# Optimization experiments

Measured on AMD Instinct MI355X. Metric: run time of the kernel, lower is better.

Reference implementation:

```python
import jax, jax.numpy as jnp
import numpy as np

NN, NB = 100_000, 20_000          # note / beat node counts
IN_C, HID, OUT_C = 64, 128, 32
NUM_LAYERS = 3
EPS_LN = 1e-5
EPS_BN = 1e-5


def setup_inputs() -> dict:
    key = jax.random.key(0)
    ks = jax.random.split(key, 24)

    def edges(k, ne, ns, nd):
        k1, k2 = jax.random.split(k)
        src = jax.random.randint(k1, (ne,), 0, ns)
        dst = jax.random.randint(k2, (ne,), 0, nd)
        return jnp.stack([src, dst]).astype(jnp.int64)

    p = lambda k, shp: jax.random.normal(k, shp, dtype=jnp.float32) * 0.05
    return {
        "x_note": jax.random.normal(ks[0], (NN, IN_C), dtype=jnp.float32),
        "x_beat": jax.random.normal(ks[1], (NB, IN_C), dtype=jnp.float32),
        "e_onset": edges(ks[2], 800_000, NN, NN),
        "e_consec": edges(ks[3], 300_000, NN, NN),
        "e_nb": edges(ks[4], 100_000, NN, NB),   # note -> beat
        "e_bn": edges(ks[5], 100_000, NB, NN),   # beat -> note
        "e_bb": edges(ks[6], 20_000, NB, NB),
        "proj_W": p(ks[7], (5, IN_C, IN_C)),
        "proj_b": jnp.zeros((5, IN_C), jnp.float32),
        "l0_Wl": p(ks[8], (5, IN_C, HID)),
        "l0_bl": jnp.zeros((5, HID), jnp.float32),
        "l0_Wr": p(ks[9], (5, IN_C, HID)),
        "Wl": p(ks[10], (NUM_LAYERS - 1, 5, HID, HID)),
        "bl": jnp.zeros((NUM_LAYERS - 1, 5, HID), jnp.float32),
        "Wr": p(ks[11], (NUM_LAYERS - 1, 5, HID, HID)),
        "ln_g": jnp.ones((NUM_LAYERS - 1, HID), jnp.float32),
        "ln_b": jnp.zeros((NUM_LAYERS - 1, HID), jnp.float32),
        "mlp_W1": p(ks[12], (HID, HID)),
        "mlp_b1": jnp.zeros((HID,), jnp.float32),
        "bn_g": jnp.ones((HID,), jnp.float32),
        "bn_b": jnp.zeros((HID,), jnp.float32),
        "mlp_W2": p(ks[13], (HID, OUT_C)),
        "mlp_b2": jnp.zeros((OUT_C,), jnp.float32),
    }


def _seg_mean(msg, dst, n):
    s = jax.ops.segment_sum(msg, dst, num_segments=n)
    c = jax.ops.segment_sum(jnp.ones((dst.shape[0], 1), msg.dtype), dst, num_segments=n)
    return s / jnp.maximum(c, 1.0)


def _l2norm(x):  # F.normalize(p=2, dim=-1)
    return x / jnp.maximum(jnp.linalg.norm(x, axis=-1, keepdims=True), 1e-12)


def _ln(x, g, b):
    m = x.mean(-1, keepdims=True)
    v = ((x - m) ** 2).mean(-1, keepdims=True)
    return (x - m) / jnp.sqrt(v + EPS_LN) * g + b


def reference(x_note, x_beat, e_onset, e_consec, e_nb, e_bn, e_bb,
              proj_W, proj_b, l0_Wl, l0_bl, l0_Wr, Wl, bl, Wr,
              ln_g, ln_b, mlp_W1, mlp_b1, bn_g, bn_b, mlp_W2, mlp_b2):
    x = {"note": x_note, "beat": x_beat}
    sizes = {"note": x_note.shape[0], "beat": x_beat.shape[0]}
    # (relation_idx, src_type, dst_type, edge_index[2,E])
    rels = [(0, "note", "note", e_onset), (1, "note", "note", e_consec),
            (2, "note", "beat", e_nb), (3, "beat", "note", e_bn),
            (4, "beat", "beat", e_bb)]

    for i in range(NUM_LAYERS):
        outs = {"note": [], "beat": []}
        for r, s, d, e in rels:
            xs, xd = x[s], x[d]
            if i == 0:  # SAGEConv(project=True, normalize=True)
                xs = jax.nn.relu(xs @ proj_W[r] + proj_b[r])
                W_l, b_l, W_r = l0_Wl[r], l0_bl[r], l0_Wr[r]
            else:
                W_l, b_l, W_r = Wl[i - 1, r], bl[i - 1, r], Wr[i - 1, r]
            agg = _seg_mean(xs[e[0]], e[1], sizes[d])       # gather -> mean scatter
            o = agg @ W_l + b_l + xd @ W_r                   # lin_l(agg) + lin_r(x_dst)
            if i == 0:
                o = _l2norm(o)
            outs[d].append(o)
        # HeteroConv aggr='mean' across relations per dst type
        x = {k: jnp.mean(jnp.stack(v), axis=0) for k, v in outs.items()}
        if i != NUM_LAYERS - 1:  # relu -> LayerNorm -> dropout(eval: identity)
            x = {k: _ln(jax.nn.relu(v), ln_g[i], ln_b[i]) for k, v in x.items()}

    note = x["note"]
    h = jax.nn.relu(note @ mlp_W1 + mlp_b1)
    # BatchNorm1d eval mode with running stats (mean=0, var=1)
    h = h / jnp.sqrt(1.0 + EPS_BN) * bn_g + bn_b
    return h @ mlp_W2 + mlp_b2
```

## Files before the change

### kernel.cpp

```cpp
#include <hip/hip_runtime.h>
#include <math.h>

typedef unsigned int   u32;
typedef unsigned short u16;
typedef short   short8 __attribute__((ext_vector_type(8)));
typedef float   f32x4  __attribute__((ext_vector_type(4)));

constexpr int NN = 100000;
constexpr int NB = 20000;
constexpr int LTOT = 3 * NN + 2 * NB;

__device__ inline float blo(u32 u) { union { u32 i; float f; } v; v.i = u << 16;        return v.f; }
__device__ inline float bhi(u32 u) { union { u32 i; float f; } v; v.i = u & 0xffff0000u; return v.f; }
__device__ inline u16  f2b(float f)
{ union { float f; u32 u; } v; v.f = f; return (u16)((v.u + 0x7fffu + ((v.u >> 16) & 1u)) >> 16); }

template<int K1, int K2, int C, int EPI, bool BIAS>
__global__ __launch_bounds__(256)
void gemm16_k(const u16* __restrict__ A1, const u16* __restrict__ A2,
              const u16* __restrict__ W, const float* __restrict__ bias,
              const float* __restrict__ g, const float* __restrict__ bvec,
              float scale, float* __restrict__ Yf, u16* __restrict__ Yh, int n)
{
    constexpr int K   = K1 + K2;
    constexpr int NKB = K / 64;
    constexpr int WVN = (C >= 64) ? 2 : 1;
    constexpr int WVM = 4 / WVN;
    constexpr int RT2 = 2;
    constexpr int BM  = WVM * RT2 * 16;
    constexpr int CT  = C / (WVN * 16);
    static_assert(K1 % 64 == 0 && (K2 == 0 || K2 % 64 == 0), "K multiple of 64");

    __shared__ uint4 sA[BM * 8];
    __shared__ uint4 sW[C * 8];
    __shared__ float redS[2][BM];
    __shared__ float redQ[2][BM];

    const int tid  = threadIdx.x;
    const int lane = tid & 63;
    const int wv   = tid >> 6;
    const int wm   = wv % WVM;
    const int wn   = wv / WVM;
    const int lrow = lane & 15;
// ... 2 lines not shown

    f32x4 acc[RT2][CT];
    #pragma unroll
    for (int rt = 0; rt < RT2; ++rt)
        #pragma unroll
        for (int ct = 0; ct < CT; ++ct) acc[rt][ct] = (f32x4){0.f, 0.f, 0.f, 0.f};

    for (int kb = 0; kb < NKB; ++kb) {
        if (kb) __syncthreads();
        const bool useA1 = (K2 == 0) || (kb * 64 < K1);
        {
            const u16* Asel   = useA1 ? A1 : A2;
            const int astride = useA1 ? K1 : K2;
            const int aoff    = useA1 ? kb * 64 : kb * 64 - K1;
            for (int u = tid; u < BM * 8; u += 256) {
                const int r  = u >> 3, k8 = u & 7;
                const int row = row0 + r;
                uint4 v = make_uint4(0u, 0u, 0u, 0u);
                if (row < n)
                    v = *reinterpret_cast<const uint4*>(Asel + (size_t)row * astride + aoff + k8 * 8);
                sA[(r * 8 + k8) ^ (r & 7)] = v;
            }
        }
        {
            u16* sWu = (u16*)sW;
            for (int u = tid; u < 64 * (C / 8); u += 256) {
                const int kk = u & 63, c8 = (u >> 6) * 8;
                const uint4 v = *reinterpret_cast<const uint4*>(W + (size_t)(kb * 64 + kk) * C + c8);
                const u16* e = (const u16*)&v;
                #pragma unroll
                for (int j = 0; j < 8; ++j) {
                    const int c = c8 + j;
                    sWu[(c * 64 + kk) ^ ((c & 7) << 3)] = e[j];
                }
            }
        }
        __syncthreads();
        #pragma unroll
        for (int ks = 0; ks < 2; ++ks) {
            short8 af[RT2];
            #pragma unroll
            for (int rt = 0; rt < RT2; ++rt) {
                const int r = (wm * RT2 + rt) * 16 + lrow;
                af[rt] = *reinterpret_cast<const short8*>(&sA[(r * 8 + ks * 4 + lk8) ^ (lrow & 7)]);
            }
            #pragma unroll
            for (int ct = 0; ct < CT; ++ct) {
                const int c = (wn * CT + ct) * 16 + lrow;
                const short8 bfr = *reinterpret_cast<const short8*>(&sW[(c * 8 + ks * 4 + lk8) ^ (lrow & 7)]);
                #pragma unroll
                for (int rt = 0; rt < RT2; ++rt)
                    acc[rt][ct] = __builtin_amdgcn_mfma_f32_16x16x32_bf16(af[rt], bfr, acc[rt][ct], 0, 0, 0);
            }
        }
    }

    float vals[RT2][CT][4];
    #pragma unroll
    for (int ct = 0; ct < CT; ++ct) {
        const int colg = (wn * CT + ct) * 16 + lrow;
        const float bs = BIAS ? bias[colg] : 0.f;
        #pragma unroll
        for (int rt = 0; rt < RT2; ++rt)
            #pragma unroll
            for (int r = 0; r < 4; ++r) {
                float v = acc[rt][ct][r] + bs;
                if (EPI == 2 || EPI == 5) v = fmaxf(v, 0.f);
                vals[rt][ct][r] = v;
            }
    }

    if (EPI <= 2) {
        #pragma unroll
        for (int ct = 0; ct < CT; ++ct) {
            const int colg = (wn * CT + ct) * 16 + lrow;
            #pragma unroll
            for (int rt = 0; rt < RT2; ++rt) {
                const int rbase = row0 + (wm * RT2 + rt) * 16 + lk8 * 4;
                #pragma unroll
                for (int r = 0; r < 4; ++r) {
                    const int row = rbase + r;
                    if (row >= n) continue;
                    if (EPI == 0) Yf[(size_t)row * C + colg] = vals[rt][ct][r];
                    else          Yh[(size_t)row * C + colg] = f2b(vals[rt][ct][r]);
                }
            }
        }
    } else {
        #pragma unroll
        for (int rt = 0; rt < RT2; ++rt)
            #pragma unroll
            for (int r = 0; r < 4; ++r) {
                float pS = 0.f, pQ = 0.f;
                #pragma unroll
                for (int ct = 0; ct < CT; ++ct) { const float v = vals[rt][ct][r]; pS += v; pQ += v * v; }
                #pragma unroll
                for (int m = 1; m <= 8; m <<= 1) {
                    pS += __shfl_xor(pS, m, 64);
                    pQ += __shfl_xor(pQ, m, 64);
                }
                if (lrow == 0) {
                    const int rowl = (wm * RT2 + rt) * 16 + lk8 * 4 + r;
                    redS[wn][rowl] = pS; redQ[wn][rowl] = pQ;
                }
            }
        __syncthreads();
        #pragma unroll
        for (int rt = 0; rt < RT2; ++rt)
            #pragma unroll
            for (int r = 0; r < 4; ++r) {
                const int rowl = (wm * RT2 + rt) * 16 + lk8 * 4 + r;
// ... 3 lines not shown
                    const float ss  = redQ[0][rowl] + redQ[1][rowl];
                    const float inv = scale / fmaxf(sqrtf(ss), 1e-12f);
                    #pragma unroll
                    for (int ct = 0; ct < CT; ++ct) {
                        const int colg = (wn * CT + ct) * 16 + lrow;
                        float o = vals[rt][ct][r] * inv;
                        if (EPI == 4) o += Yf[(size_t)row * C + colg];
                        Yf[(size_t)row * C + colg] = o;
                    }
                } else {
                    const float S = redS[0][rowl] + redS[1][rowl];
                    const float Q = redQ[0][rowl] + redQ[1][rowl];
                    const float mean = S * (1.0f / C);
                    const float var  = Q * (1.0f / C) - mean * mean;
                    const float inv  = 1.0f / sqrtf(var + 1e-5f);
                    #pragma unroll
                    for (int ct = 0; ct < CT; ++ct) {
                        const int colg = (wn * CT + ct) * 16 + lrow;
                        const float o = (vals[rt][ct][r] - mean) * inv * g[colg] + bvec[colg];
                        Yh[(size_t)row * C + colg] = f2b(o);
                    }
                }
            }
    }
}

struct Rels { const int* e[5]; int E[5]; int rowoff[5]; };

__global__ __launch_bounds__(256)
void hist_all_k(Rels R, int* __restrict__ deg)
{
    const int ri = blockIdx.y;
    const int e = blockIdx.x * 256 + threadIdx.x;
    if (e < R.E[ri]) atomicAdd(&deg[R.rowoff[ri] + R.e[ri][e + R.E[ri]]], 1);
}

__global__ __launch_bounds__(256)
void fill_all_k(Rels R, const int* __restrict__ rowptr, int* __restrict__ next,
                int* __restrict__ colsrc)
{
    const int ri = blockIdx.y;
    const int e = blockIdx.x * 256 + threadIdx.x;
    if (e >= R.E[ri]) return;
    const int s = R.e[ri][e], d = R.e[ri][e + R.E[ri]];
    const int p = atomicAdd(&next[R.rowoff[ri] + d], 1);
    colsrc[rowptr[R.rowoff[ri] + d] + p] = s;
// ... 38 lines not shown
    #pragma unroll
    for (int off = 1; off < 64; off <<= 1) {
        const int u = __shfl_up(sc, off, 64);
        if ((tid & 63) >= off) sc += u;
    }
    if ((tid & 63) == 63) ws[tid >> 6] = sc;
    __syncthreads();
    int add = 0;
    for (int i = 0; i < (tid >> 6); ++i) add += ws[i];
    if (tid < nb) bsum[tid] = sc + add;
}

__global__ __launch_bounds__(256)
void scan3_k(int* __restrict__ rowptr, const int* __restrict__ bsum, int n)
{
    const int i = blockIdx.x * 256 + threadIdx.x;
    if (i == 0) rowptr[0] = 0;
    if (i < n) {
        const int b = i >> 11;
        if (b > 0) rowptr[i + 1] += bsum[b - 1];
    }
}

__global__ __launch_bounds__(256)
void agg128_k(const u16* __restrict__ X, const int* __restrict__ rowptr,
              const int* __restrict__ colsrc, int rowoff, int n, float scale,
              u16* __restrict__ out, int rs, int co)
{
    const int wid  = (int)((blockIdx.x * 256 + threadIdx.x) >> 6);
    const int lane = threadIdx.x & 63;
    if (wid >= n) return;
    const int beg = rowptr[rowoff + wid], end = rowptr[rowoff + wid + 1];
    const int sub = lane >> 5, cl = lane & 31;
    const uint2* X2 = (const uint2*)X;
    float a0 = 0.f, a1 = 0.f, a2 = 0.f, a3 = 0.f;
    int j = beg + sub;
    for (; j + 2 < end; j += 4) {
        const int s0 = colsrc[j], s1 = colsrc[j + 2];
        const uint2 v0 = X2[(size_t)s0 * 32 + cl];
        const uint2 v1 = X2[(size_t)s1 * 32 + cl];
        a0 += blo(v0.x) + blo(v1.x); a1 += bhi(v0.x) + bhi(v1.x);
        a2 += blo(v0.y) + blo(v1.y); a3 += bhi(v0.y) + bhi(v1.y);
    }
    for (; j < end; j += 2) {
        const uint2 v = X2[(size_t)colsrc[j] * 32 + cl];
        a0 += blo(v.x); a1 += bhi(v.x); a2 += blo(v.y); a3 += bhi(v.y);
    }
    a0 += __shfl_xor(a0, 32, 64); a1 += __shfl_xor(a1, 32, 64);
    a2 += __shfl_xor(a2, 32, 64); a3 += __shfl_xor(a3, 32, 64);
    if (sub == 0) {
        const float m = scale / fmaxf((float)(end - beg), 1.0f);
        uint2 p;
        p.x = (u32)f2b(a0 * m) | ((u32)f2b(a1 * m) << 16);
        p.y = (u32)f2b(a2 * m) | ((u32)f2b(a3 * m) << 16);
        ((uint2*)(out + (size_t)wid * rs + co))[cl] = p;
    }
}

__global__ __launch_bounds__(256)
void agg64_k(const u16* __restrict__ X, const int* __restrict__ rowptr,
             const int* __restrict__ colsrc, int rowoff, int n, float scale,
             u16* __restrict__ out)
{
    const int wid  = (int)((blockIdx.x * 256 + threadIdx.x) >> 6);
    const int lane = threadIdx.x & 63;
    if (wid >= n) return;
    const int beg = rowptr[rowoff + wid], end = rowptr[rowoff + wid + 1];
    const int sub = lane >> 5, cl = lane & 31;
    const u32* X1 = (const u32*)X;
    float a0 = 0.f, a1 = 0.f;
    int j = beg + sub;
    for (; j + 2 < end; j += 4) {
        const u32 v0 = X1[(size_t)colsrc[j] * 32 + cl];
        const u32 v1 = X1[(size_t)colsrc[j + 2] * 32 + cl];
        a0 += blo(v0) + blo(v1); a1 += bhi(v0) + bhi(v1);
    }
    for (; j < end; j += 2) {
        const u32 v = X1[(size_t)colsrc[j] * 32 + cl];
        a0 += blo(v); a1 += bhi(v);
    }
    a0 += __shfl_xor(a0, 32, 64); a1 += __shfl_xor(a1, 32, 64);
    if (sub == 0) {
        const float m = scale / fmaxf((float)(end - beg), 1.0f);
        ((u32*)(out + (size_t)wid * 64))[cl] = (u32)f2b(a0 * m) | ((u32)f2b(a1 * m) << 16);
    }
}

__global__ __launch_bounds__(256)
void relu_ln16_k(const float* __restrict__ X, const float* __restrict__ g,
                 const float* __restrict__ b, u16* __restrict__ OUT, int n)
{
    const int wid  = (int)((blockIdx.x * 256 + threadIdx.x) >> 6);
    const int lane = threadIdx.x & 63;
    if (wid >= n) return;
    const float* x = X + (size_t)wid * 128;
    const float v0 = fmaxf(x[lane], 0.f), v1 = fmaxf(x[lane + 64], 0.f);
    float s = v0 + v1;
    #pragma unroll
    for (int off = 32; off > 0; off >>= 1) s += __shfl_xor(s, off, 64);
    const float m  = s * (1.0f / 128.0f);
    const float d0 = v0 - m, d1 = v1 - m;
    float vv = d0 * d0 + d1 * d1;
    #pragma unroll
    for (int off = 32; off > 0; off >>= 1) vv += __shfl_xor(vv, off, 64);
    const float inv = 1.0f / sqrtf(vv * (1.0f / 128.0f) + 1e-5f);
    OUT[(size_t)wid * 128 + lane]      = f2b(d0 * inv * g[lane]      + b[lane]);
    OUT[(size_t)wid * 128 + lane + 64] = f2b(d1 * inv * g[lane + 64] + b[lane + 64]);
}

__global__ void l0wcat_k(const float* __restrict__ Wl, const float* __restrict__ Wr,
                         u16* __restrict__ out)
{
    const int r = blockIdx.y;
    const int idx = blockIdx.x * 256 + threadIdx.x;
    const int row = idx >> 7, c = idx & 127;
    const float v = (row < 64) ? Wl[(size_t)r * 8192 + row * 128 + c]
                               : Wr[(size_t)r * 8192 + (row - 64) * 128 + c];
    out[(size_t)r * 16384 + idx] = f2b(v);
}

__global__ void wcat_k(const float* __restrict__ Wl, const float* __restrict__ Wr,
                       const float* __restrict__ bl, u16* __restrict__ WcatN,
                       u16* __restrict__ WcatB, float* __restrict__ bcatN,
                       float* __restrict__ bcatB)
{
    const int job = blockIdx.y;
    const int idx = blockIdx.x * 256 + threadIdx.x;
    if (job < 2) {
        const int li = job;
        const float* WlL = Wl + (size_t)li * 5 * 16384;
        const float* WrL = Wr + (size_t)li * 5 * 16384;
        if (idx < 512 * 128) {
            const int row = idx >> 7, c = idx & 127;
            float v;
            if (row < 384) {
                const int rsel = row >> 7;
                const int rel = (rsel == 2) ? 3 : rsel;
                v = WlL[(size_t)rel * 16384 + (row & 127) * 128 + c];
            } else {
                const int rr = row - 384;
                v = (WrL[(size_t)0 * 16384 + rr * 128 + c] + WrL[(size_t)1 * 16384 + rr * 128 + c]
                   + WrL[(size_t)3 * 16384 + rr * 128 + c]) * (1.0f / 3.0f);
            }
            WcatN[(size_t)li * 512 * 128 + idx] = f2b(v);
        }
        if (blockIdx.x == 0 && threadIdx.x < 128) {
            const float* blL = bl + (size_t)li * 5 * 128;
            bcatN[li * 128 + threadIdx.x] =
                (blL[threadIdx.x] + blL[128 + threadIdx.x] + blL[3 * 128 + threadIdx.x]) * (1.0f / 3.0f);
        }
    } else {
        if (idx < 384 * 128) {
            const int row = idx >> 7, c = idx & 127;
            float v;
            if (row < 256) {
                const int rel = (row < 128) ? 2 : 4;
                v = Wl[(size_t)rel * 16384 + (row & 127) * 128 + c];
            } else {
                const int rr = row - 256;
                v = (Wr[(size_t)2 * 16384 + rr * 128 + c] + Wr[(size_t)4 * 16384 + rr * 128 + c]) * 0.5f;
            }
            WcatB[idx] = f2b(v);
        }
        if (blockIdx.x == 0 && threadIdx.x < 128)
            bcatB[threadIdx.x] = (bl[2 * 128 + threadIdx.x] + bl[4 * 128 + threadIdx.x]) * 0.5f;
    }
}

__global__ void headprep_k(const float* __restrict__ W2, const float* __restrict__ b2,
                           const float* __restrict__ bng, const float* __restrict__ bnb,
                           u16* __restrict__ W2p16, float* __restrict__ b2p)
{
    const int idx = blockIdx.x * 256 + threadIdx.x;
    const float is = 1.0f / sqrtf(1.0f + 1e-5f);
    if (idx < 128 * 32) {
        const int k = idx >> 5;
        W2p16[idx] = f2b(W2[idx] * (bng[k] * is));
    }
    if (idx < 32) {
        float s = b2[idx];
        for (int k = 0; k < 128; ++k) s += bnb[k] * W2[k * 32 + idx];
        b2p[idx] = s;
    }
}

struct CastJobs { const float* s[4]; u16* d[4]; int n[4]; };
__global__ __launch_bounds__(256)
void castmany_k(CastJobs J)
{
    const int j = blockIdx.y;
    const float* s = J.s[j]; u16* d = J.d[j]; const int n = J.n[j];
    for (int i = blockIdx.x * 256 + threadIdx.x; i < n; i += gridDim.x * 256)
        d[i] = f2b(s[i]);
}

extern "C" void kernel_launch(void* const* d_in, const int* in_sizes, int n_in,
                              void* d_out, int out_size, void* d_ws, size_t ws_size,
                              hipStream_t stream)
{
    (void)n_in; (void)out_size; (void)ws_size;

    const float* x_note = (const float*)d_in[0];
    const float* x_beat = (const float*)d_in[1];
    const int*   e_on   = (const int*)d_in[2];
    const int*   e_co   = (const int*)d_in[3];
    const int*   e_nb   = (const int*)d_in[4];
    const int*   e_bn   = (const int*)d_in[5];
    const int*   e_bb   = (const int*)d_in[6];
    const float* proj_W = (const float*)d_in[7];
    const float* proj_b = (const float*)d_in[8];
    const float* l0_Wl  = (const float*)d_in[9];
    const float* l0_bl  = (const float*)d_in[10];
    const float* l0_Wr  = (const float*)d_in[11];
    const float* Wl     = (const float*)d_in[12];
    const float* bl     = (const float*)d_in[13];
    const float* Wr     = (const float*)d_in[14];
    const float* ln_g   = (const float*)d_in[15];
    const float* ln_b   = (const float*)d_in[16];
    const float* W1     = (const float*)d_in[17];
    const float* b1     = (const float*)d_in[18];
    const float* bn_g   = (const float*)d_in[19];
    const float* bn_b   = (const float*)d_in[20];
    const float* W2     = (const float*)d_in[21];
    const float* b2     = (const float*)d_in[22];

    const int E_on = in_sizes[2] / 2, E_co = in_sizes[3] / 2, E_nb = in_sizes[4] / 2,
              E_bn = in_sizes[5] / 2, E_bb = in_sizes[6] / 2;
    const int ETOT = E_on + E_co + E_nb + E_bn + E_bb;

    char* wsb = (char*)d_ws;
    size_t off = 0;
    auto alloc = [&](size_t bytes) { char* p = wsb + off; off += (bytes + 255) & ~(size_t)255; return p; };
    float* nF    = (float*)alloc((size_t)NN * 128 * 4);
    float* bF    = (float*)alloc((size_t)NB * 128 * 4);
    u16*  n16    = (u16*)alloc((size_t)NN * 128 * 2);
    u16*  b16    = (u16*)alloc((size_t)NB * 128 * 2);
    u16*  agg16  = (u16*)alloc((size_t)NN * 384 * 2);
    u16*  aggB   = (u16*)alloc((size_t)NB * 256 * 2);
    u16*  xn16   = n16;
    u16*  xb16   = b16;
    u16*  n16h   = (u16*)nF;
    u16*  proj16 = agg16 + (size_t)NN * 64;
    u16*  tmp16h = agg16;
    u16*  projW16 = (u16*)alloc(5 * 64 * 64 * 2);
    u16*  l0Wc16  = (u16*)alloc(5 * 128 * 128 * 2);
    u16*  WcatN   = (u16*)alloc(2 * 512 * 128 * 2);
    u16*  WcatB   = (u16*)alloc(384 * 128 * 2);
    u16*  W116    = (u16*)alloc(128 * 128 * 2);
    u16*  W2p16   = (u16*)alloc(128 * 32 * 2);
    float* bcatN  = (float*)alloc(2 * 128 * 4);
    float* bcatB  = (float*)alloc(128 * 4);
    float* b2p    = (float*)alloc(32 * 4);
    int* rowptr = (int*)alloc((LTOT + 64) * 4);
    int* deg    = (int*)alloc(LTOT * 4);
    int* colsrc = (int*)alloc((size_t)ETOT * 4);
    int* bsum   = (int*)alloc(256 * 4);

    Rels R;
    R.e[0] = e_on; R.e[1] = e_co; R.e[2] = e_nb; R.e[3] = e_bn; R.e[4] = e_bb;
    R.E[0] = E_on; R.E[1] = E_co; R.E[2] = E_nb; R.E[3] = E_bn; R.E[4] = E_bb;
    R.rowoff[0] = 0; R.rowoff[1] = NN; R.rowoff[2] = 2 * NN;
    R.rowoff[3] = 2 * NN + NB; R.rowoff[4] = 3 * NN + NB;
    int maxE = E_on;
    for (int i = 1; i < 5; ++i) if (R.E[i] > maxE) maxE = R.E[i];

    hipMemsetAsync(deg, 0, (size_t)LTOT * 4, stream);
    hist_all_k<<<dim3((maxE + 255) / 256, 5), 256, 0, stream>>>(R, deg);
    const int NBLK = (LTOT + 2047) / 2048;
    scan1_k<<<NBLK, 256, 0, stream>>>(deg, rowptr, bsum, LTOT);
    scan2p_k<<<1, 256, 0, stream>>>(bsum, NBLK);
    scan3_k<<<(LTOT + 255) / 256, 256, 0, stream>>>(rowptr, bsum, LTOT);
    hipMemsetAsync(deg, 0, (size_t)LTOT * 4, stream);
    fill_all_k<<<dim3((maxE + 255) / 256, 5), 256, 0, stream>>>(R, rowptr, deg, colsrc);

    l0wcat_k<<<dim3(64, 5), 256, 0, stream>>>(l0_Wl, l0_Wr, l0Wc16);
    wcat_k<<<dim3(256, 3), 256, 0, stream>>>(Wl, Wr, bl, WcatN, WcatB, bcatN, bcatB);
    headprep_k<<<16, 256, 0, stream>>>(W2, b2, bn_g, bn_b, W2p16, b2p);
    {
        CastJobs J;
        J.s[0] = x_note; J.d[0] = xn16;    J.n[0] = NN * 64;
        J.s[1] = x_beat; J.d[1] = xb16;    J.n[1] = NB * 64;
        J.s[2] = proj_W; J.d[2] = projW16; J.n[2] = 5 * 64 * 64;
        J.s[3] = W1;     J.d[3] = W116;    J.n[3] = 128 * 128;
        castmany_k<<<dim3(512, 4), 256, 0, stream>>>(J);
    }

    const int nsz[2] = {NN, NB};
    const int  relS[5] = {0, 0, 0, 1, 1};
    const int  relD[5] = {0, 0, 1, 0, 1};
    const float Rdiv[2] = {3.0f, 2.0f};

    for (int ri = 0; ri < 5; ++ri) {
        const u16* xs = relS[ri] == 0 ? xn16 : xb16;
        const u16* xd = relD[ri] == 0 ? xn16 : xb16;
        const int ns = nsz[relS[ri]], nd = nsz[relD[ri]];
        float* accum = relD[ri] == 0 ? nF : bF;
        const float sc = 1.0f / Rdiv[relD[ri]];
        gemm16_k<64, 0, 64, 2, true><<<(ns + 63) / 64, 256, 0, stream>>>(
            xs, nullptr, projW16 + (size_t)ri * 4096, proj_b + ri * 64,
            nullptr, nullptr, 0.f, nullptr, proj16, ns);
        agg64_k<<<(nd + 3) / 4, 256, 0, stream>>>(proj16, rowptr, colsrc, R.rowoff[ri], nd, 1.0f, agg16);
        if (ri == 0 || ri == 2)
            gemm16_k<64, 64, 128, 3, true><<<(nd + 63) / 64, 256, 0, stream>>>(
                agg16, xd, l0Wc16 + (size_t)ri * 16384, l0_bl + ri * 128,
                nullptr, nullptr, sc, accum, nullptr, nd);
        else
            gemm16_k<64, 64, 128, 4, true><<<(nd + 63) / 64, 256, 0, stream>>>(
                agg16, xd, l0Wc16 + (size_t)ri * 16384, l0_bl + ri * 128,
                nullptr, nullptr, sc, accum, nullptr, nd);
    }
    relu_ln16_k<<<(NN + 3) / 4, 256, 0, stream>>>(nF, ln_g, ln_b, n16, NN);
    relu_ln16_k<<<(NB + 3) / 4, 256, 0, stream>>>(bF, ln_g, ln_b, b16, NB);

    agg128_k<<<(NN + 3) / 4, 256, 0, stream>>>(n16, rowptr, colsrc, 0,            NN, 1.0f / 3.0f, agg16, 384, 0);
    agg128_k<<<(NN + 3) / 4, 256, 0, stream>>>(n16, rowptr, colsrc, NN,           NN, 1.0f / 3.0f, agg16, 384, 128);
    agg128_k<<<(NN + 3) / 4, 256, 0, stream>>>(b16, rowptr, colsrc, 2 * NN + NB,  NN, 1.0f / 3.0f, agg16, 384, 256);
    agg128_k<<<(NB + 3) / 4, 256, 0, stream>>>(n16, rowptr, colsrc, 2 * NN,       NB, 0.5f,        aggB, 256, 0);
    agg128_k<<<(NB + 3) / 4, 256, 0, stream>>>(b16, rowptr, colsrc, 3 * NN + NB,  NB, 0.5f,        aggB, 256, 128);
    gemm16_k<384, 128, 128, 5, true><<<(NN + 63) / 64, 256, 0, stream>>>(
        agg16, n16, WcatN, bcatN, ln_g + 128, ln_b + 128, 0.f, nullptr, n16, NN);
    gemm16_k<256, 128, 128, 5, true><<<(NB + 63) / 64, 256, 0, stream>>>(
        aggB, b16, WcatB, bcatB, ln_g + 128, ln_b + 128, 0.f, nullptr, b16, NB);

    agg128_k<<<(NN + 3) / 4, 256, 0, stream>>>(n16, rowptr, colsrc, 0,            NN, 1.0f / 3.0f, agg16, 384, 0);
    agg128_k<<<(NN + 3) / 4, 256, 0, stream>>>(n16, rowptr, colsrc, NN,           NN, 1.0f / 3.0f, agg16, 384, 128);
    agg128_k<<<(NN + 3) / 4, 256, 0, stream>>>(b16, rowptr, colsrc, 2 * NN + NB,  NN, 1.0f / 3.0f, agg16, 384, 256);
    gemm16_k<384, 128, 128, 1, true><<<(NN + 63) / 64, 256, 0, stream>>>(
        agg16, n16, WcatN + 512 * 128, bcatN + 128, nullptr, nullptr, 0.f, nullptr, n16h, NN);

    gemm16_k<128, 0, 128, 2, true><<<(NN + 63) / 64, 256, 0, stream>>>(
        n16h, nullptr, W116, b1, nullptr, nullptr, 0.f, nullptr, tmp16h, NN);
    gemm16_k<128, 0, 32, 0, true><<<(NN + 127) / 128, 256, 0, stream>>>(
        tmp16h, nullptr, W2p16, b2p, nullptr, nullptr, 0.f, (float*)d_out, nullptr, NN);
}
```

Measured before the change: 913.2 us.

## Pre-swizzle weights, batch projections and aggregations, fuse relu+LayerNorm into GEMM epilogue

Weights are pre-swizzled once into the shared-memory layout, so the GEMM loads B tiles with plain 16-byte copies instead of scattered 2-byte stores. The per-relation layer-0 projections are merged into one wide GEMM per source type. All per-relation aggregations of a layer now run as a single multi-job kernel instead of separate launches. A new epilogue folds L2-normalise, accumulate, relu and LayerNorm into the last layer-0 GEMM, which removes the standalone relu_ln passes. The trade-off is more launch-table indexing inside the aggregation kernel and a heavier epilogue with extra barriers.

Result: slower. 938.8 us (+2.8%).

```diff
diff --git a/kernel.cpp b/kernel.cpp
--- a/kernel.cpp
+++ b/kernel.cpp
@@ -18,7 +18,7 @@
 template<int K1, int K2, int C, int EPI, bool BIAS>
 __global__ __launch_bounds__(256)
 void gemm16_k(const u16* __restrict__ A1, const u16* __restrict__ A2,
-              const u16* __restrict__ W, const float* __restrict__ bias,
+              const uint4* __restrict__ Wsw, const float* __restrict__ bias,
               const float* __restrict__ g, const float* __restrict__ bvec,
               float scale, float* __restrict__ Yf, u16* __restrict__ Yh, int n)
 {
@@ -67,19 +67,8 @@
                 sA[(r * 8 + k8) ^ (r & 7)] = v;
             }
         }
-        {
-            u16* sWu = (u16*)sW;
-            for (int u = tid; u < 64 * (C / 8); u += 256) {
-                const int kk = u & 63, c8 = (u >> 6) * 8;
-                const uint4 v = *reinterpret_cast<const uint4*>(W + (size_t)(kb * 64 + kk) * C + c8);
-                const u16* e = (const u16*)&v;
-                #pragma unroll
-                for (int j = 0; j < 8; ++j) {
-                    const int c = c8 + j;
-                    sWu[(c * 64 + kk) ^ ((c & 7) << 3)] = e[j];
-                }
-            }
-        }
+        for (int u = tid; u < C * 8; u += 256)
+            sW[u] = Wsw[(size_t)kb * C * 8 + u];
         __syncthreads();
         #pragma unroll
         for (int ks = 0; ks < 2; ++ks) {
@@ -92,7 +81,7 @@
             #pragma unroll
             for (int ct = 0; ct < CT; ++ct) {
                 const int c = (wn * CT + ct) * 16 + lrow;
-                const short8 bfr = *reinterpret_cast<const short8*>(&sW[(c * 8 + ks * 4 + lk8) ^ (lrow & 7)]);
+                const short8 bfr = *reinterpret_cast<const short8*>(&sW[(c * 8 + ks * 4 + lk8) ^ (c & 7)]);
                 #pragma unroll
                 for (int rt = 0; rt < RT2; ++rt)
                     acc[rt][ct] = __builtin_amdgcn_mfma_f32_16x16x32_bf16(af[rt], bfr, acc[rt][ct], 0, 0, 0);
@@ -131,7 +120,7 @@
                 }
             }
         }
-    } else {
+    } else if (EPI == 3 || EPI == 4 || EPI == 5) {
         #pragma unroll
         for (int rt = 0; rt < RT2; ++rt)
             #pragma unroll
@@ -181,6 +170,73 @@
                     }
                 }
             }
+    } else {
+        #pragma unroll
+        for (int rt = 0; rt < RT2; ++rt)
+            #pragma unroll
+            for (int r = 0; r < 4; ++r) {
+                float pQ = 0.f;
+                #pragma unroll
+                for (int ct = 0; ct < CT; ++ct) { const float v = vals[rt][ct][r]; pQ += v * v; }
+                #pragma unroll
+                for (int m = 1; m <= 8; m <<= 1) pQ += __shfl_xor(pQ, m, 64);
+                if (lrow == 0) redQ[wn][(wm * RT2 + rt) * 16 + lk8 * 4 + r] = pQ;
+            }
+        __syncthreads();
+        #pragma unroll
+        for (int rt = 0; rt < RT2; ++rt)
+            #pragma unroll
+            for (int r = 0; r < 4; ++r) {
+                const int rowl = (wm * RT2 + rt) * 16 + lk8 * 4 + r;
+                const int row = row0 + rowl;
+                const float ss  = redQ[0][rowl] + redQ[1][rowl];
+                const float inv = scale / fmaxf(sqrtf(ss), 1e-12f);
+                #pragma unroll
+                for (int ct = 0; ct < CT; ++ct) {
+                    const int colg = (wn * CT + ct) * 16 + lrow;
+                    float o = vals[rt][ct][r] * inv;
+                    if (row < n) o += Yf[(size_t)row * C + colg];
+                    vals[rt][ct][r] = fmaxf(o, 0.f);
+                }
+            }
+        __syncthreads();
+        #pragma unroll
+        for (int rt = 0; rt < RT2; ++rt)
+            #pragma unroll
+            for (int r = 0; r < 4; ++r) {
+                float pS = 0.f, pQ = 0.f;
+                #pragma unroll
+                for (int ct = 0; ct < CT; ++ct) { const float v = vals[rt][ct][r]; pS += v; pQ += v * v; }
+                #pragma unroll
+                for (int m = 1; m <= 8; m <<= 1) {
+                    pS += __shfl_xor(pS, m, 64);
+                    pQ += __shfl_xor(pQ, m, 64);
+                }
+                if (lrow == 0) {
+                    const int rowl = (wm * RT2 + rt) * 16 + lk8 * 4 + r;
+                    redS[wn][rowl] = pS; redQ[wn][rowl] = pQ;
+                }
+            }
+        __syncthreads();
+        #pragma unroll
+        for (int rt = 0; rt < RT2; ++rt)
+            #pragma unroll
+            for (int r = 0; r < 4; ++r) {
+                const int rowl = (wm * RT2 + rt) * 16 + lk8 * 4 + r;
+                const int row = row0 + rowl;
+                if (row >= n) continue;
+                const float S = redS[0][rowl] + redS[1][rowl];
+                const float Q = redQ[0][rowl] + redQ[1][rowl];
+                const float mean = S * (1.0f / C);
+                const float var  = Q * (1.0f / C) - mean * mean;
+                const float inv  = 1.0f / sqrtf(var + 1e-5f);
+                #pragma unroll
+                for (int ct = 0; ct < CT; ++ct) {
+                    const int colg = (wn * CT + ct) * 16 + lrow;
+                    const float o = (vals[rt][ct][r] - mean) * inv * g[colg] + bvec[colg];
+                    Yh[(size_t)row * C + colg] = f2b(o);
+                }
+            }
     }
 }
 
@@ -265,176 +321,186 @@
     }
 }
 
-__global__ __launch_bounds__(256)
-void agg128_k(const u16* __restrict__ X, const int* __restrict__ rowptr,
-              const int* __restrict__ colsrc, int rowoff, int n, float scale,
-              u16* __restrict__ out, int rs, int co)
-{
-    const int wid  = (int)((blockIdx.x * 256 + threadIdx.x) >> 6);
+struct AggJobs {
+    const u16* X[5];
+    u16* out[5];
+    int in_rs[5], in_co[5], rowoff[5], nrows[5], out_rs[5], out_co[5];
+    float scale[5];
+    int pfx[6];
+    int njobs;
+};
+
+template<int C>
+__global__ __launch_bounds__(256)
+void aggm_k(AggJobs J, const int* __restrict__ rowptr, const int* __restrict__ colsrc)
+{
+    const int bid = blockIdx.x;
+    int j = 0;
+    while (j + 1 < J.njobs && bid >= J.pfx[j + 1]) ++j;
+    const int wid = (bid - J.pfx[j]) * 4 + (int)(threadIdx.x >> 6);
+    if (wid >= J.nrows[j]) return;
     const int lane = threadIdx.x & 63;
-    if (wid >= n) return;
-    const int beg = rowptr[rowoff + wid], end = rowptr[rowoff + wid + 1];
     const int sub = lane >> 5, cl = lane & 31;
-    const uint2* X2 = (const uint2*)X;
-    float a0 = 0.f, a1 = 0.f, a2 = 0.f, a3 = 0.f;
-    int j = beg + sub;
-    for (; j + 2 < end; j += 4) {
-        const int s0 = colsrc[j], s1 = colsrc[j + 2];
-        const uint2 v0 = X2[(size_t)s0 * 32 + cl];
-        const uint2 v1 = X2[(size_t)s1 * 32 + cl];
-        a0 += blo(v0.x) + blo(v1.x); a1 += bhi(v0.x) + bhi(v1.x);
-        a2 += blo(v0.y) + blo(v1.y); a3 += bhi(v0.y) + bhi(v1.y);
-    }
-    for (; j < end; j += 2) {
-        const uint2 v = X2[(size_t)colsrc[j] * 32 + cl];
-        a0 += blo(v.x); a1 += bhi(v.x); a2 += blo(v.y); a3 += bhi(v.y);
-    }
-    a0 += __shfl_xor(a0, 32, 64); a1 += __shfl_xor(a1, 32, 64);
-    a2 += __shfl_xor(a2, 32, 64); a3 += __shfl_xor(a3, 32, 64);
-    if (sub == 0) {
-        const float m = scale / fmaxf((float)(end - beg), 1.0f);
-        uint2 p;
-        p.x = (u32)f2b(a0 * m) | ((u32)f2b(a1 * m) << 16);
-        p.y = (u32)f2b(a2 * m) | ((u32)f2b(a3 * m) << 16);
-        ((uint2*)(out + (size_t)wid * rs + co))[cl] = p;
-    }
-}
-
-__global__ __launch_bounds__(256)
-void agg64_k(const u16* __restrict__ X, const int* __restrict__ rowptr,
-             const int* __restrict__ colsrc, int rowoff, int n, float scale,
-             u16* __restrict__ out)
-{
-    const int wid  = (int)((blockIdx.x * 256 + threadIdx.x) >> 6);
-    const int lane = threadIdx.x & 63;
-    if (wid >= n) return;
-    const int beg = rowptr[rowoff + wid], end = rowptr[rowoff + wid + 1];
-    const int sub = lane >> 5, cl = lane & 31;
-    const u32* X1 = (const u32*)X;
-    float a0 = 0.f, a1 = 0.f;
-    int j = beg + sub;
-    for (; j + 2 < end; j += 4) {
-        const u32 v0 = X1[(size_t)colsrc[j] * 32 + cl];
-        const u32 v1 = X1[(size_t)colsrc[j + 2] * 32 + cl];
-        a0 += blo(v0) + blo(v1); a1 += bhi(v0) + bhi(v1);
-    }
-    for (; j < end; j += 2) {
-        const u32 v = X1[(size_t)colsrc[j] * 32 + cl];
-        a0 += blo(v); a1 += bhi(v);
-    }
-    a0 += __shfl_xor(a0, 32, 64); a1 += __shfl_xor(a1, 32, 64);
-    if (sub == 0) {
-        const float m = scale / fmaxf((float)(end - beg), 1.0f);
-        ((u32*)(out + (size_t)wid * 64))[cl] = (u32)f2b(a0 * m) | ((u32)f2b(a1 * m) << 16);
-    }
-}
-
-__global__ __launch_bounds__(256)
-void relu_ln16_k(const float* __restrict__ X, const float* __restrict__ g,
-                 const float* __restrict__ b, u16* __restrict__ OUT, int n)
-{
-    const int wid  = (int)((blockIdx.x * 256 + threadIdx.x) >> 6);
-    const int lane = threadIdx.x & 63;
-    if (wid >= n) return;
-    const float* x = X + (size_t)wid * 128;
-    const float v0 = fmaxf(x[lane], 0.f), v1 = fmaxf(x[lane + 64], 0.f);
-    float s = v0 + v1;
+    const int beg = rowptr[J.rowoff[j] + wid], end = rowptr[J.rowoff[j] + wid + 1];
+    const u16* X = J.X[j];
+    const int irs = J.in_rs[j], ico = J.in_co[j];
+    const float m = J.scale[j] / fmaxf((float)(end - beg), 1.0f);
+    if (C == 128) {
+        float a0 = 0.f, a1 = 0.f, a2 = 0.f, a3 = 0.f;
+        int i = beg + sub;
+        for (; i + 2 < end; i += 4) {
+            const int s0 = colsrc[i], s1 = colsrc[i + 2];
+            const uint2 v0 = *reinterpret_cast<const uint2*>(X + (size_t)s0 * irs + ico + cl * 4);
+            const uint2 v1 = *reinterpret_cast<const uint2*>(X + (size_t)s1 * irs + ico + cl * 4);
+            a0 += blo(v0.x) + blo(v1.x); a1 += bhi(v0.x) + bhi(v1.x);
+            a2 += blo(v0.y) + blo(v1.y); a3 += bhi(v0.y) + bhi(v1.y);
+        }
+        for (; i < end; i += 2) {
+            const uint2 v = *reinterpret_cast<const uint2*>(X + (size_t)colsrc[i] * irs + ico + cl * 4);
+            a0 += blo(v.x); a1 += bhi(v.x); a2 += blo(v.y); a3 += bhi(v.y);
+        }
+        a0 += __shfl_xor(a0, 32, 64); a1 += __shfl_xor(a1, 32, 64);
+        a2 += __shfl_xor(a2, 32, 64); a3 += __shfl_xor(a3, 32, 64);
+        if (sub == 0) {
+            uint2 p;
+            p.x = (u32)f2b(a0 * m) | ((u32)f2b(a1 * m) << 16);
+            p.y = (u32)f2b(a2 * m) | ((u32)f2b(a3 * m) << 16);
+            *reinterpret_cast<uint2*>(J.out[j] + (size_t)wid * J.out_rs[j] + J.out_co[j] + cl * 4) = p;
+        }
+    } else {
+        float a0 = 0.f, a1 = 0.f;
+        int i = beg + sub;
+        for (; i + 2 < end; i += 4) {
+            const u32 v0 = *reinterpret_cast<const u32*>(X + (size_t)colsrc[i] * irs + ico + cl * 2);
+            const u32 v1 = *reinterpret_cast<const u32*>(X + (size_t)colsrc[i + 2] * irs + ico + cl * 2);
+            a0 += blo(v0) + blo(v1); a1 += bhi(v0) + bhi(v1);
+        }
+        for (; i < end; i += 2) {
+            const u32 v = *reinterpret_cast<const u32*>(X + (size_t)colsrc[i] * irs + ico + cl * 2);
+            a0 += blo(v); a1 += bhi(v);
+        }
+        a0 += __shfl_xor(a0, 32, 64); a1 += __shfl_xor(a1, 32, 64);
+        if (sub == 0)
+            *reinterpret_cast<u32*>(J.out[j] + (size_t)wid * J.out_rs[j] + J.out_co[j] + cl * 2) =
+                (u32)f2b(a0 * m) | ((u32)f2b(a1 * m) << 16);
+    }
+}
+
+__global__ __launch_bounds__(256)
+void wprep_k(const float* __restrict__ proj_W, const float* __restrict__ l0_Wl,
+             const float* __restrict__ l0_Wr, const float* __restrict__ Wl,
+             const float* __restrict__ Wr, const float* __restrict__ W1,
+             const float* __restrict__ W2, const float* __restrict__ bn_g,
+             uint4* __restrict__ projNsw, uint4* __restrict__ projBsw,
+             uint4* __restrict__ l0Wsw, uint4* __restrict__ WcatNsw,
+             uint4* __restrict__ WcatBsw, uint4* __restrict__ W1sw,
+             uint4* __restrict__ W2sw)
+{
+    const int job = blockIdx.y;
+    const int t = blockIdx.x * 256 + threadIdx.x;
+    int K, C; uint4* dst;
+    switch (job) {
+        case 0:  K = 64;  C = 192; dst = projNsw; break;
+        case 1:  K = 64;  C = 128; dst = projBsw; break;
+        case 2: case 3: case 4: case 5: case 6:
+                 K = 128; C = 128; dst = l0Wsw + (size_t)(job - 2) * 2048; break;
+        case 7: case 8:
+                 K = 512; C = 128; dst = WcatNsw + (size_t)(job - 7) * 8192; break;
+        case 9:  K = 384; C = 128; dst = WcatBsw; break;
+        case 10: K = 128; C = 128; dst = W1sw; break;
+        default: K = 128; C = 32;  dst = W2sw; break;
+    }
+    if (t >= K * C / 8) return;
+    const int kb = t / (C * 8);
+    const int rem = t % (C * 8);
+    const int c = rem >> 3, k8 = rem & 7;
+    const int k0 = kb * 64 + k8 * 8;
+    const float is = 1.0f / sqrtf(1.0f + 1e-5f);
+    u16 e[8];
     #pragma unroll
-    for (int off = 32; off > 0; off >>= 1) s += __shfl_xor(s, off, 64);
-    const float m  = s * (1.0f / 128.0f);
-    const float d0 = v0 - m, d1 = v1 - m;
-    float vv = d0 * d0 + d1 * d1;
-    #pragma unroll
-    for (int off = 32; off > 0; off >>= 1) vv += __shfl_xor(vv, off, 64);
-    const float inv = 1.0f / sqrtf(vv * (1.0f / 128.0f) + 1e-5f);
-    OUT[(size_t)wid * 128 + lane]      = f2b(d0 * inv * g[lane]      + b[lane]);
-    OUT[(size_t)wid * 128 + lane + 64] = f2b(d1 * inv * g[lane + 64] + b[lane + 64]);
-}
-
-__global__ void l0wcat_k(const float* __restrict__ Wl, const float* __restrict__ Wr,
-                         u16* __restrict__ out)
-{
-    const int r = blockIdx.y;
-    const int idx = blockIdx.x * 256 + threadIdx.x;
-    const int row = idx >> 7, c = idx & 127;
-    const float v = (row < 64) ? Wl[(size_t)r * 8192 + row * 128 + c]
-                               : Wr[(size_t)r * 8192 + (row - 64) * 128 + c];
-    out[(size_t)r * 16384 + idx] = f2b(v);
-}
-
-__global__ void wcat_k(const float* __restrict__ Wl, const float* __restrict__ Wr,
-                       const float* __restrict__ bl, u16* __restrict__ WcatN,
-                       u16* __restrict__ WcatB, float* __restrict__ bcatN,
-                       float* __restrict__ bcatB)
-{
-    const int job = blockIdx.y;
-    const int idx = blockIdx.x * 256 + threadIdx.x;
-    if (job < 2) {
-        const int li = job;
-        const float* WlL = Wl + (size_t)li * 5 * 16384;
-        const float* WrL = Wr + (size_t)li * 5 * 16384;
-        if (idx < 512 * 128) {
-            const int row = idx >> 7, c = idx & 127;
-            float v;
-            if (row < 384) {
-                const int rsel = row >> 7;
-                const int rel = (rsel == 2) ? 3 : rsel;
-                v = WlL[(size_t)rel * 16384 + (row & 127) * 128 + c];
-            } else {
-                const int rr = row - 384;
-                v = (WrL[(size_t)0 * 16384 + rr * 128 + c] + WrL[(size_t)1 * 16384 + rr * 128 + c]
-                   + WrL[(size_t)3 * 16384 + rr * 128 + c]) * (1.0f / 3.0f);
-            }
-            WcatN[(size_t)li * 512 * 128 + idx] = f2b(v);
-        }
-        if (blockIdx.x == 0 && threadIdx.x < 128) {
-            const float* blL = bl + (size_t)li * 5 * 128;
-            bcatN[li * 128 + threadIdx.x] =
-                (blL[threadIdx.x] + blL[128 + threadIdx.x] + blL[3 * 128 + threadIdx.x]) * (1.0f / 3.0f);
-        }
+    for (int jj = 0; jj < 8; ++jj) {
+        const int k = k0 + jj;
+        float v;
+        switch (job) {
+            case 0:  v = proj_W[(size_t)(c >> 6) * 4096 + k * 64 + (c & 63)]; break;
+            case 1:  v = proj_W[(size_t)(3 + (c >> 6)) * 4096 + k * 64 + (c & 63)]; break;
+            case 2: case 3: case 4: case 5: case 6: {
+                const int r = job - 2;
+                v = (k < 64) ? l0_Wl[(size_t)r * 8192 + k * 128 + c]
+                             : l0_Wr[(size_t)r * 8192 + (k - 64) * 128 + c];
+                break;
+            }
+            case 7: case 8: {
+                const int li = job - 7;
+                const float* WlL = Wl + (size_t)li * 5 * 16384;
+                const float* WrL = Wr + (size_t)li * 5 * 16384;
+                if (k < 384) {
+                    const int sel = k >> 7;
+                    const int rel = (sel == 2) ? 3 : sel;
+                    v = WlL[(size_t)rel * 16384 + (k & 127) * 128 + c];
+                } else {
+                    const int rr = k - 384;
+                    v = (WrL[(size_t)rr * 128 + c] + WrL[16384 + (size_t)rr * 128 + c]
+                       + WrL[3 * 16384 + (size_t)rr * 128 + c]) * (1.0f / 3.0f);
+                }
+                break;
+            }
+            case 9: {
+                if (k < 256) {
+                    const int rel = (k < 128) ? 2 : 4;
+                    v = Wl[(size_t)rel * 16384 + (k & 127) * 128 + c];
+                } else {
+                    const int rr = k - 256;
+                    v = (Wr[2 * 16384 + (size_t)rr * 128 + c] + Wr[4 * 16384 + (size_t)rr * 128 + c]) * 0.5f;
+                }
+                break;
+            }
+            case 10: v = W1[(size_t)k * 128 + c]; break;
+            default: v = W2[(size_t)k * 32 + c] * (bn_g[k] * is); break;
+        }
+        e[jj] = f2b(v);
+    }
+    uint4 p;
+    p.x = (u32)e[0] | ((u32)e[1] << 16);
+    p.y = (u32)e[2] | ((u32)e[3] << 16);
+    p.z = (u32)e[4] | ((u32)e[5] << 16);
+    p.w = (u32)e[6] | ((u32)e[7] << 16);
+    dst[(size_t)kb * C * 8 + ((c * 8 + k8) ^ (c & 7))] = p;
+}
+
+__global__ __launch_bounds__(512)
+void biasprep_k(const float* __restrict__ bl, const float* __restrict__ b2,
+                const float* __restrict__ bn_b, const float* __restrict__ W2,
+                float* __restrict__ bcatN, float* __restrict__ bcatB,
+                float* __restrict__ b2p)
+{
+    const int t = threadIdx.x;
+    if (t < 256) {
+        const int li = t >> 7, c = t & 127;
+        const float* blL = bl + (size_t)li * 640;
+        bcatN[t] = (blL[c] + blL[128 + c] + blL[384 + c]) * (1.0f / 3.0f);
+    } else if (t < 384) {
+        const int c = t - 256;
+        bcatB[c] = (bl[256 + c] + bl[512 + c]) * 0.5f;
+    } else if (t < 416) {
+        const int c = t - 384;
+        float s = b2[c];
+        for (int k = 0; k < 128; ++k) s += bn_b[k] * W2[k * 32 + c];
+        b2p[c] = s;
+    }
+}
+
+__global__ __launch_bounds__(256)
+void castfeat_k(const float* __restrict__ xn, const float* __restrict__ xb,
+                u16* __restrict__ dn, u16* __restrict__ db)
+{
+    if (blockIdx.y == 0) {
+        for (int i = blockIdx.x * 256 + threadIdx.x; i < NN * 64; i += gridDim.x * 256)
+            dn[i] = f2b(xn[i]);
     } else {
-        if (idx < 384 * 128) {
-            const int row = idx >> 7, c = idx & 127;
-            float v;
-            if (row < 256) {
-                const int rel = (row < 128) ? 2 : 4;
-                v = Wl[(size_t)rel * 16384 + (row & 127) * 128 + c];
-            } else {
-                const int rr = row - 256;
-                v = (Wr[(size_t)2 * 16384 + rr * 128 + c] + Wr[(size_t)4 * 16384 + rr * 128 + c]) * 0.5f;
-            }
-            WcatB[idx] = f2b(v);
-        }
-        if (blockIdx.x == 0 && threadIdx.x < 128)
-            bcatB[threadIdx.x] = (bl[2 * 128 + threadIdx.x] + bl[4 * 128 + threadIdx.x]) * 0.5f;
-    }
-}
-
-__global__ void headprep_k(const float* __restrict__ W2, const float* __restrict__ b2,
-                           const float* __restrict__ bng, const float* __restrict__ bnb,
-                           u16* __restrict__ W2p16, float* __restrict__ b2p)
-{
-    const int idx = blockIdx.x * 256 + threadIdx.x;
-    const float is = 1.0f / sqrtf(1.0f + 1e-5f);
-    if (idx < 128 * 32) {
-        const int k = idx >> 5;
-        W2p16[idx] = f2b(W2[idx] * (bng[k] * is));
-    }
-    if (idx < 32) {
-        float s = b2[idx];
-        for (int k = 0; k < 128; ++k) s += bnb[k] * W2[k * 32 + idx];
-        b2p[idx] = s;
-    }
-}
-
-struct CastJobs { const float* s[4]; u16* d[4]; int n[4]; };
-__global__ __launch_bounds__(256)
-void castmany_k(CastJobs J)
-{
-    const int j = blockIdx.y;
-    const float* s = J.s[j]; u16* d = J.d[j]; const int n = J.n[j];
-    for (int i = blockIdx.x * 256 + threadIdx.x; i < n; i += gridDim.x * 256)
-        d[i] = f2b(s[i]);
+        for (int i = blockIdx.x * 256 + threadIdx.x; i < NB * 64; i += gridDim.x * 256)
+            db[i] = f2b(xb[i]);
+    }
 }
 
 extern "C" void kernel_launch(void* const* d_in, const int* in_sizes, int n_in,
@@ -474,28 +540,33 @@
     char* wsb = (char*)d_ws;
     size_t off = 0;
     auto alloc = [&](size_t bytes) { char* p = wsb + off; off += (bytes + 255) & ~(size_t)255; return p; };
-    float* nF    = (float*)alloc((size_t)NN * 128 * 4);
-    float* bF    = (float*)alloc((size_t)NB * 128 * 4);
-    u16*  n16    = (u16*)alloc((size_t)NN * 128 * 2);
-    u16*  b16    = (u16*)alloc((size_t)NB * 128 * 2);
-    u16*  agg16  = (u16*)alloc((size_t)NN * 384 * 2);
-    u16*  aggB   = (u16*)alloc((size_t)NB * 256 * 2);
-    u16*  xn16   = n16;
-    u16*  xb16   = b16;
-    u16*  n16h   = (u16*)nF;
-    u16*  proj16 = agg16 + (size_t)NN * 64;
-    u16*  tmp16h = agg16;
-    u16*  projW16 = (u16*)alloc(5 * 64 * 64 * 2);
-    u16*  l0Wc16  = (u16*)alloc(5 * 128 * 128 * 2);
-    u16*  WcatN   = (u16*)alloc(2 * 512 * 128 * 2);
-    u16*  WcatB   = (u16*)alloc(384 * 128 * 2);
-    u16*  W116    = (u16*)alloc(128 * 128 * 2);
-    u16*  W2p16   = (u16*)alloc(128 * 32 * 2);
-    float* bcatN  = (float*)alloc(2 * 128 * 4);
-    float* bcatB  = (float*)alloc(128 * 4);
-    float* b2p    = (float*)alloc(32 * 4);
-    int* rowptr = (int*)alloc((LTOT + 64) * 4);
-    int* deg    = (int*)alloc(LTOT * 4);
+    char* R1 = alloc((size_t)NN * 128 * 4 + (size_t)NB * 128 * 4 + (size_t)(3 * NN + 2 * NB) * 64 * 2);
+    float* nF    = (float*)R1;
+    float* bF    = (float*)(R1 + (size_t)NN * 128 * 4);
+    u16*  aggL0  = (u16*)(R1 + (size_t)NN * 128 * 4 + (size_t)NB * 128 * 4);
+    u16*  agg16  = (u16*)R1;
+    u16*  aggB   = (u16*)(R1 + (size_t)NN * 384 * 2);
+    u16*  tmp16h = (u16*)R1;
+    char* R2 = alloc((size_t)NN * 192 * 2 + (size_t)NB * 128 * 2);
+    u16*  projN = (u16*)R2;
+    u16*  projB = (u16*)(R2 + (size_t)NN * 192 * 2);
+    u16*  n16h  = (u16*)R2;
+    u16*  xn16 = (u16*)alloc((size_t)NN * 64 * 2);
+    u16*  xb16 = (u16*)alloc((size_t)NB * 64 * 2);
+    u16*  n16  = (u16*)alloc((size_t)NN * 128 * 2);
+    u16*  b16  = (u16*)alloc((size_t)NB * 128 * 2);
+    uint4* projNsw = (uint4*)alloc(1536 * 16);
+    uint4* projBsw = (uint4*)alloc(1024 * 16);
+    uint4* l0Wsw   = (uint4*)alloc(5 * 2048 * 16);
+    uint4* WcatNsw = (uint4*)alloc(2 * 8192 * 16);
+    uint4* WcatBsw = (uint4*)alloc(6144 * 16);
+    uint4* W1sw    = (uint4*)alloc(2048 * 16);
+    uint4* W2sw    = (uint4*)alloc(512 * 16);
+    float* bcatN   = (float*)alloc(2 * 128 * 4);
+    float* bcatB   = (float*)alloc(128 * 4);
+    float* b2p     = (float*)alloc(32 * 4);
+    int* rowptr = (int*)alloc((size_t)(LTOT + 64) * 4);
+    int* deg    = (int*)alloc((size_t)LTOT * 4);
     int* colsrc = (int*)alloc((size_t)ETOT * 4);
     int* bsum   = (int*)alloc(256 * 4);
 
@@ -516,63 +587,90 @@
     hipMemsetAsync(deg, 0, (size_t)LTOT * 4, stream);
     fill_all_k<<<dim3((maxE + 255) / 256, 5), 256, 0, stream>>>(R, rowptr, deg, colsrc);
 
-    l0wcat_k<<<dim3(64, 5), 256, 0, stream>>>(l0_Wl, l0_Wr, l0Wc16);
-    wcat_k<<<dim3(256, 3), 256, 0, stream>>>(Wl, Wr, bl, WcatN, WcatB, bcatN, bcatB);
-    headprep_k<<<16, 256, 0, stream>>>(W2, b2, bn_g, bn_b, W2p16, b2p);
+    wprep_k<<<dim3(32, 12), 256, 0, stream>>>(proj_W, l0_Wl, l0_Wr, Wl, Wr, W1, W2, bn_g,
+                                              projNsw, projBsw, l0Wsw, WcatNsw, WcatBsw, W1sw, W2sw);
+    biasprep_k<<<1, 512, 0, stream>>>(bl, b2, bn_b, W2, bcatN, bcatB, b2p);
+    castfeat_k<<<dim3(512, 2), 256, 0, stream>>>(x_note, x_beat, xn16, xb16);
+
+    u16* aL0[5] = { aggL0,
+                    aggL0 + (size_t)NN * 64,
+                    aggL0 + (size_t)2 * NN * 64,
+                    aggL0 + (size_t)2 * NN * 64 + (size_t)NB * 64,
+                    aggL0 + (size_t)3 * NN * 64 + (size_t)NB * 64 };
+
+    gemm16_k<64, 0, 192, 2, true><<<(NN + 63) / 64, 256, 0, stream>>>(
+        xn16, nullptr, projNsw, proj_b, nullptr, nullptr, 0.f, nullptr, projN, NN);
+    gemm16_k<64, 0, 128, 2, true><<<(NB + 63) / 64, 256, 0, stream>>>(
+        xb16, nullptr, projBsw, proj_b + 192, nullptr, nullptr, 0.f, nullptr, projB, NB);
     {
-        CastJobs J;
-        J.s[0] = x_note; J.d[0] = xn16;    J.n[0] = NN * 64;
-        J.s[1] = x_beat; J.d[1] = xb16;    J.n[1] = NB * 64;
-        J.s[2] = proj_W; J.d[2] = projW16; J.n[2] = 5 * 64 * 64;
-        J.s[3] = W1;     J.d[3] = W116;    J.n[3] = 128 * 128;
-        castmany_k<<<dim3(512, 4), 256, 0, stream>>>(J);
-    }
-
-    const int nsz[2] = {NN, NB};
-    const int  relS[5] = {0, 0, 0, 1, 1};
-    const int  relD[5] = {0, 0, 1, 0, 1};
-    const float Rdiv[2] = {3.0f, 2.0f};
-
-    for (int ri = 0; ri < 5; ++ri) {
-        const u16* xs = relS[ri] == 0 ? xn16 : xb16;
-        const u16* xd = relD[ri] == 0 ? xn16 : xb16;
-        const int ns = nsz[relS[ri]], nd = nsz[relD[ri]];
-        float* accum = relD[ri] == 0 ? nF : bF;
-        const float sc = 1.0f / Rdiv[relD[ri]];
-        gemm16_k<64, 0, 64, 2, true><<<(ns + 63) / 64, 256, 0, stream>>>(
-            xs, nullptr, projW16 + (size_t)ri * 4096, proj_b + ri * 64,
-            nullptr, nullptr, 0.f, nullptr, proj16, ns);
-        agg64_k<<<(nd + 3) / 4, 256, 0, stream>>>(proj16, rowptr, colsrc, R.rowoff[ri], nd, 1.0f, agg16);
-        if (ri == 0 || ri == 2)
-            gemm16_k<64, 64, 128, 3, true><<<(nd + 63) / 64, 256, 0, stream>>>(
-                agg16, xd, l0Wc16 + (size_t)ri * 16384, l0_bl + ri * 128,
-                nullptr, nullptr, sc, accum, nullptr, nd);
-        else
-            gemm16_k<64, 64, 128, 4, true><<<(nd + 63) / 64, 256, 0, stream>>>(
-                agg16, xd, l0Wc16 + (size_t)ri * 16384, l0_bl + ri * 128,
-                nullptr, nullptr, sc, accum, nullptr, nd);
-    }
-    relu_ln16_k<<<(NN + 3) / 4, 256, 0, stream>>>(nF, ln_g, ln_b, n16, NN);
-    relu_ln16_k<<<(NB + 3) / 4, 256, 0, stream>>>(bF, ln_g, ln_b, b16, NB);
-
-    agg128_k<<<(NN + 3) / 4, 256, 0, stream>>>(n16, rowptr, colsrc, 0,            NN, 1.0f / 3.0f, agg16, 384, 0);
-    agg128_k<<<(NN + 3) / 4, 256, 0, stream>>>(n16, rowptr, colsrc, NN,           NN, 1.0f / 3.0f, agg16, 384, 128);
-    agg128_k<<<(NN + 3) / 4, 256, 0, stream>>>(b16, rowptr, colsrc, 2 * NN + NB,  NN, 1.0f / 3.0f, agg16, 384, 256);
-    agg128_k<<<(NB + 3) / 4, 256, 0, stream>>>(n16, rowptr, colsrc, 2 * NN,       NB, 0.5f,        aggB, 256, 0);
-    agg128_k<<<(NB + 3) / 4, 256, 0, stream>>>(b16, rowptr, colsrc, 3 * NN + NB,  NB, 0.5f,        aggB, 256, 128);
+        AggJobs J; J.njobs = 5;
+        const u16* Xs[5]  = {projN, projN, projN, projB, projB};
+        const int  irs[5] = {192, 192, 192, 128, 128};
+        const int  ico[5] = {0, 64, 128, 0, 64};
+        const int  ro[5]  = {0, NN, 2 * NN, 2 * NN + NB, 3 * NN + NB};
+        const int  nr[5]  = {NN, NN, NB, NN, NB};
+        J.pfx[0] = 0;
+        for (int q = 0; q < 5; ++q) {
+            J.X[q] = Xs[q]; J.in_rs[q] = irs[q]; J.in_co[q] = ico[q];
+            J.rowoff[q] = ro[q]; J.nrows[q] = nr[q];
+            J.out[q] = aL0[q]; J.out_rs[q] = 64; J.out_co[q] = 0; J.scale[q] = 1.0f;
+            J.pfx[q + 1] = J.pfx[q] + (nr[q] + 3) / 4;
+        }
+        aggm_k<64><<<J.pfx[5], 256, 0, stream>>>(J, rowptr, colsrc);
+    }
+    gemm16_k<64, 64, 128, 3, true><<<(NN + 63) / 64, 256, 0, stream>>>(
+        aL0[0], xn16, l0Wsw, l0_bl, nullptr, nullptr, 1.0f / 3.0f, nF, nullptr, NN);
+    gemm16_k<64, 64, 128, 4, true><<<(NN + 63) / 64, 256, 0, stream>>>(
+        aL0[1], xn16, l0Wsw + 2048, l0_bl + 128, nullptr, nullptr, 1.0f / 3.0f, nF, nullptr, NN);
+    gemm16_k<64, 64, 128, 3, true><<<(NB + 63) / 64, 256, 0, stream>>>(
+        aL0[2], xb16, l0Wsw + 2 * 2048, l0_bl + 2 * 128, nullptr, nullptr, 0.5f, bF, nullptr, NB);
+    gemm16_k<64, 64, 128, 6, true><<<(NN + 63) / 64, 256, 0, stream>>>(
+        aL0[3], xn16, l0Wsw + 3 * 2048, l0_bl + 3 * 128, ln_g, ln_b, 1.0f / 3.0f, nF, n16, NN);
+    gemm16_k<64, 64, 128, 6, true><<<(NB + 63) / 64, 256, 0, stream>>>(
+        aL0[4], xb16, l0Wsw + 4 * 2048, l0_bl + 4 * 128, ln_g, ln_b, 0.5f, bF, b16, NB);
+
+    {
+        AggJobs J; J.njobs = 5;
+        const u16* Xs[5]  = {n16, n16, b16, n16, b16};
+        const int  ro[5]  = {0, NN, 2 * NN + NB, 2 * NN, 3 * NN + NB};
+        const int  nr[5]  = {NN, NN, NN, NB, NB};
+        u16* outs[5]      = {agg16, agg16, agg16, aggB, aggB};
+        const int ors[5]  = {384, 384, 384, 256, 256};
+        const int oco[5]  = {0, 128, 256, 0, 128};
+        const float sc[5] = {1.0f / 3, 1.0f / 3, 1.0f / 3, 0.5f, 0.5f};
+        J.pfx[0] = 0;
+        for (int q = 0; q < 5; ++q) {
+            J.X[q] = Xs[q]; J.in_rs[q] = 128; J.in_co[q] = 0;
+            J.rowoff[q] = ro[q]; J.nrows[q] = nr[q];
+            J.out[q] = outs[q]; J.out_rs[q] = ors[q]; J.out_co[q] = oco[q]; J.scale[q] = sc[q];
+            J.pfx[q + 1] = J.pfx[q] + (nr[q] + 3) / 4;
+        }
+        aggm_k<128><<<J.pfx[5], 256, 0, stream>>>(J, rowptr, colsrc);
+    }
     gemm16_k<384, 128, 128, 5, true><<<(NN + 63) / 64, 256, 0, stream>>>(
-        agg16, n16, WcatN, bcatN, ln_g + 128, ln_b + 128, 0.f, nullptr, n16, NN);
+        agg16, n16, WcatNsw, bcatN, ln_g + 128, ln_b + 128, 0.f, nullptr, n16, NN);
     gemm16_k<256, 128, 128, 5, true><<<(NB + 63) / 64, 256, 0, stream>>>(
-        aggB, b16, WcatB, bcatB, ln_g + 128, ln_b + 128, 0.f, nullptr, b16, NB);
-
-    agg128_k<<<(NN + 3) / 4, 256, 0, stream>>>(n16, rowptr, colsrc, 0,            NN, 1.0f / 3.0f, agg16, 384, 0);
-    agg128_k<<<(NN + 3) / 4, 256, 0, stream>>>(n16, rowptr, colsrc, NN,           NN, 1.0f / 3.0f, agg16, 384, 128);
-    agg128_k<<<(NN + 3) / 4, 256, 0, stream>>>(b16, rowptr, colsrc, 2 * NN + NB,  NN, 1.0f / 3.0f, agg16, 384, 256);
+        aggB, b16, WcatBsw, bcatB, ln_g + 128, ln_b + 128, 0.f, nullptr, b16, NB);
+
+    {
+        AggJobs J; J.njobs = 3;
+        const u16* Xs[3] = {n16, n16, b16};
+        const int  ro[3] = {0, NN, 2 * NN + NB};
+        const int  oco[3] = {0, 128, 256};
+        J.pfx[0] = 0;
+        for (int q = 0; q < 3; ++q) {
+            J.X[q] = Xs[q]; J.in_rs[q] = 128; J.in_co[q] = 0;
+            J.rowoff[q] = ro[q]; J.nrows[q] = NN;
+            J.out[q] = agg16; J.out_rs[q] = 384; J.out_co[q] = oco[q]; J.scale[q] = 1.0f / 3.0f;
+            J.pfx[q + 1] = J.pfx[q] + (NN + 3) / 4;
+        }
+        aggm_k<128><<<J.pfx[3], 256, 0, stream>>>(J, rowptr, colsrc);
+    }
     gemm16_k<384, 128, 128, 1, true><<<(NN + 63) / 64, 256, 0, stream>>>(
-        agg16, n16, WcatN + 512 * 128, bcatN + 128, nullptr, nullptr, 0.f, nullptr, n16h, NN);
+        agg16, n16, WcatNsw + 8192, bcatN + 128, nullptr, nullptr, 0.f, nullptr, n16h, NN);
 
     gemm16_k<128, 0, 128, 2, true><<<(NN + 63) / 64, 256, 0, stream>>>(
-        n16h, nullptr, W116, b1, nullptr, nullptr, 0.f, nullptr, tmp16h, NN);
+        n16h, nullptr, W1sw, b1, nullptr, nullptr, 0.f, nullptr, tmp16h, NN);
     gemm16_k<128, 0, 32, 0, true><<<(NN + 127) / 128, 256, 0, stream>>>(
-        tmp16h, nullptr, W2p16, b2p, nullptr, nullptr, 0.f, (float*)d_out, nullptr, NN);
-}
+        tmp16h, nullptr, W2sw, b2p, nullptr, nullptr, 0.f, (float*)d_out, nullptr, NN);
+}
```
